# Performance work log

Hardware: AMD Instinct MI355X
Metric: run time of the kernel (lower is better)

## Reference

```python
import jax, jax.numpy as jnp
import numpy as np

B, T, H, D = 1, 2048, 32, 64
SCALE = 0.015625  # 1/64 = 1/head_size
DEG = 2


def setup_inputs() -> dict:
    key = jax.random.key(0)
    k1, k2, k3, k4 = jax.random.split(key, 4)
    q = jax.random.normal(k1, (B, T, H, D), dtype=jnp.float32)
    k = jax.random.normal(k2, (B, T, H, D), dtype=jnp.float32)
    v = jax.random.normal(k3, (B, T, H, D), dtype=jnp.float32)
    # log_G: per-token, per-head log decay (must be <= 0)
    g = -0.1 * jax.random.uniform(k4, (B, T, H), dtype=jnp.float32)
    return {"q": q, "k": k, "v": v, "g": g}


def reference(q, k, v, g):
    # q,k,v: [B,T,H,D]; g: [B,T,H] log-decay (log_G)
    # Power retention, deg=2, attention (quadratic) form for T <= switch_over_seq_len.
    g_cum = jnp.cumsum(g, axis=1)                         # [B,T,H]
    gc = jnp.transpose(g_cum, (0, 2, 1))                  # [B,H,T]
    # decay weight exp(gc[t]-gc[s]) for s<=t, 0 otherwise
    log_decay = gc[:, :, :, None] - gc[:, :, None, :]     # [B,H,T,S]
    causal = jnp.tril(jnp.ones((T, T), dtype=bool))
    decay = jnp.where(causal, jnp.exp(log_decay), 0.0)    # [B,H,T,S]
    qk = jnp.einsum("bthd,bshd->bhts", q, k) * SCALE      # [B,H,T,S]
    w = (qk ** DEG) * decay                               # nonneg scores, deg=2
    num = jnp.einsum("bhts,bshd->bthd", w, v)             # [B,T,H,D]
    denom = jnp.transpose(w.sum(-1), (0, 2, 1))           # [B,T,H]
    out = num / jnp.maximum(denom, 1.0)[..., None]
    return out
```

## Files before the change

kernel.cpp:

```cpp
#include <hip/hip_runtime.h>

#define T_DIM 2048
#define H_DIM 32
#define D_DIM 64
#define SCALE_F 0.015625f
#define TILE_STRIDE 2048

typedef unsigned short ushort;
typedef __attribute__((ext_vector_type(8))) short short8;
typedef __attribute__((ext_vector_type(16))) float f32x16;

__global__ __launch_bounds__(256)
void cumsum_g_kernel(const float* __restrict__ g, float* __restrict__ gc) {
    const int h = blockIdx.x;
    const int tid = threadIdx.x;
    const int PER = T_DIM / 256;

    __shared__ float sums[256];

    float loc[8];
    float run = 0.f;
    const int t0 = tid * PER;
    for (int i = 0; i < PER; ++i) {
        run += g[(size_t)(t0 + i) * H_DIM + h];
        loc[i] = run;
    }
    sums[tid] = run;
    __syncthreads();

    for (int off = 1; off < 256; off <<= 1) {
        float vv = (tid >= off) ? sums[tid - off] : 0.f;
        __syncthreads();
        sums[tid] += vv;
        __syncthreads();
    }
    float excl = (tid == 0) ? 0.f : sums[tid - 1];

    for (int i = 0; i < PER; ++i)
        gc[(size_t)h * T_DIM + t0 + i] = excl + loc[i];
}

__device__ __forceinline__ ushort f2bf(float x) {
    unsigned u = __float_as_uint(x);
    unsigned r = (u + 0x7fffu + ((u >> 16) & 1u)) >> 16;
    return (ushort)r;
}

__global__ __launch_bounds__(256)
void prep_kernel(const float* __restrict__ q, const float* __restrict__ k,
                 const float* __restrict__ v, const float* __restrict__ gc,
                 ushort* __restrict__ qfrag, ushort* __restrict__ kfrag,
                 ushort* __restrict__ vfrag) {
    __shared__ ushort qt_l[64 * 64];
    __shared__ ushort kt_l[64 * 64];

    const int h   = blockIdx.x;
    const int tt  = blockIdx.y;
    const int tid = threadIdx.x;

    {
        const int r    = tid >> 2;
        const int dseg = (tid & 3) * 16;
        const int t    = tt * 64 + r;
        const float gct = gc[(size_t)h * T_DIM + t];
        const float eq = SCALE_F * __expf(0.5f * gct);
        const float ek = __expf(-0.5f * gct);
        const float* qp = q + ((size_t)t * H_DIM + h) * 64 + dseg;
        const float* kp = k + ((size_t)t * H_DIM + h) * 64 + dseg;
        union { ushort u[16]; uint4 uu[2]; } oq, ok;
#pragma unroll
        for (int i = 0; i < 16; ++i) {
            oq.u[i] = f2bf(qp[i] * eq);
            ok.u[i] = f2bf(kp[i] * ek);
        }
        const int c0 = (tid & 3) * 2;
#pragma unroll
        for (int cc = 0; cc < 2; ++cc) {
            const int slot = (c0 + cc) ^ (r & 7);
            *reinterpret_cast<uint4*>(&qt_l[r * 64 + slot * 8]) = oq.uu[cc];
            *reinterpret_cast<uint4*>(&kt_l[r * 64 + slot * 8]) = ok.uu[cc];
        }
    }
    __syncthreads();

#pragma unroll
    for (int n = 0; n < 2; ++n) {
        const int ch   = tid + 256 * n;
        const int l31  = ch & 31;
        const int hi   = (ch >> 5) & 1;
        const int ks   = (ch >> 6) & 3;
        const int t32r = ch >> 8;
        const int row  = t32r * 32 + l31;
        const int slot = (2 * ks + hi) ^ (row & 7);
        uint4 qq = *reinterpret_cast<const uint4*>(&qt_l[row * 64 + slot * 8]);
        uint4 kk = *reinterpret_cast<const uint4*>(&kt_l[row * 64 + slot * 8]);
        const size_t base = ((size_t)h * 64 + tt * 2 + t32r) * TILE_STRIDE
                          + (size_t)(((ks * 2 + hi) * 32) + l31) * 8;
        *reinterpret_cast<uint4*>(qfrag + base) = qq;
        *reinterpret_cast<uint4*>(kfrag + base) = kk;
    }

#pragma unroll
    for (int n = 0; n < 2; ++n) {
        const int c9   = (tid >> 5) + 8 * n;
        const int l31  = tid & 31;
        const int hi   = c9 & 1;
        const int kh2  = (c9 >> 1) & 1;
        const int dblk = (c9 >> 2) & 1;
        const int s32r = c9 >> 3;
        const int tb = tt * 64 + s32r * 32 + kh2 * 16 + hi * 8;
        union { ushort u[8]; uint4 uu; } ov;
#pragma unroll
        for (int j = 0; j < 8; ++j)
            ov.u[j] = f2bf(v[((size_t)(tb + j) * H_DIM + h) * 64 + dblk * 32 + l31]);
        const size_t base = ((size_t)h * 64 + tt * 2 + s32r) * TILE_STRIDE
                          + (size_t)((((dblk * 2 + kh2) * 2 + hi) * 32) + l31) * 8;
        *reinterpret_cast<uint4*>(vfrag + base) = ov.uu;
    }
}

__device__ __forceinline__ short8 ld8(const ushort* p) {
    return *reinterpret_cast<const short8*>(p);
}

__device__ __forceinline__ unsigned cvt_pk_bf16(float lo, float hi) {
    unsigned r;
    asm("v_cvt_pk_bf16_f32 %0, %1, %2" : "=v"(r) : "v"(lo), "v"(hi));
    return r;
}

__device__ __forceinline__ short8 pack_w(const float* w8) {
    unsigned p0 = cvt_pk_bf16(w8[0], w8[1]);
    unsigned p1 = cvt_pk_bf16(w8[2], w8[3]);
    unsigned p2 = cvt_pk_bf16(w8[4], w8[5]);
    unsigned p3 = cvt_pk_bf16(w8[6], w8[7]);
    asm("v_permlane32_swap_b32 %0, %1" : "+v"(p0), "+v"(p2));
    asm("v_permlane32_swap_b32 %0, %1" : "+v"(p1), "+v"(p3));
    union { unsigned u[4]; short8 s; } af;
    af.u[0] = p0; af.u[1] = p1; af.u[2] = p2; af.u[3] = p3;
    return af.s;
}

template<int MODE>
__device__ __forceinline__ void step64(
    const ushort* __restrict__ kb, const ushort* __restrict__ vb,
    int lofs, int hi, int l31,
    const short8 (&qrL)[4], const short8 (&qrH)[4],
    f32x16& o00, f32x16& o01, f32x16& o10, f32x16& o11,
    float& denL, float& denH)
{
    const short8 vf00 = ld8(vb + lofs);
    const short8 vf10 = ld8(vb + 512 + lofs);
    const short8 vf01 = ld8(vb + 1024 + lofs);
    const short8 vf11 = ld8(vb + 1536 + lofs);
    const short8 kf0 = ld8(kb + lofs);
    const short8 kf1 = ld8(kb + 512 + lofs);
    const short8 kf2 = ld8(kb + 1024 + lofs);
    const short8 kf3 = ld8(kb + 1536 + lofs);

    f32x16 cH;
#pragma unroll
    for (int i = 0; i < 16; ++i) cH[i] = 0.f;
    f32x16 cL = cH;

    if (MODE <= 1) {
        cL = __builtin_amdgcn_mfma_f32_32x32x16_bf16(kf0, qrL[0], cL, 0, 0, 0);
        cH = __builtin_amdgcn_mfma_f32_32x32x16_bf16(kf0, qrH[0], cH, 0, 0, 0);
        cL = __builtin_amdgcn_mfma_f32_32x32x16_bf16(kf1, qrL[1], cL, 0, 0, 0);
        cH = __builtin_amdgcn_mfma_f32_32x32x16_bf16(kf1, qrH[1], cH, 0, 0, 0);
        cL = __builtin_amdgcn_mfma_f32_32x32x16_bf16(kf2, qrL[2], cL, 0, 0, 0);
        cH = __builtin_amdgcn_mfma_f32_32x32x16_bf16(kf2, qrH[2], cH, 0, 0, 0);
        cL = __builtin_amdgcn_mfma_f32_32x32x16_bf16(kf3, qrL[3], cL, 0, 0, 0);
        cH = __builtin_amdgcn_mfma_f32_32x32x16_bf16(kf3, qrH[3], cH, 0, 0, 0);
    } else {
        cH = __builtin_amdgcn_mfma_f32_32x32x16_bf16(kf0, qrH[0], cH, 0, 0, 0);
        cH = __builtin_amdgcn_mfma_f32_32x32x16_bf16(kf1, qrH[1], cH, 0, 0, 0);
        cH = __builtin_amdgcn_mfma_f32_32x32x16_bf16(kf2, qrH[2], cH, 0, 0, 0);
        cH = __builtin_amdgcn_mfma_f32_32x32x16_bf16(kf3, qrH[3], cH, 0, 0, 0);
    }

    float wL[16], wH[16];
#pragma unroll
    for (int r = 0; r < 16; ++r) {
        const int s_local = (r & 3) + 8 * (r >> 2) + 4 * hi;
        float xh = cH[r];
        float wwh = xh * xh;
        if (MODE == 2) wwh = (s_local <= l31) ? wwh : 0.f;
        wH[r] = wwh;
        denH += wwh;
        if (MODE <= 1) {
            float xl = cL[r];
            float wwl = xl * xl;
            if (MODE == 1) wwl = (s_local <= l31) ? wwl : 0.f;
            wL[r] = wwl;
            denL += wwl;
        }
    }

    if (MODE <= 1) {
        const short8 a0 = pack_w(&wL[0]);
        o00 = __builtin_amdgcn_mfma_f32_32x32x16_bf16(a0, vf00, o00, 0, 0, 0);
        o01 = __builtin_amdgcn_mfma_f32_32x32x16_bf16(a0, vf01, o01, 0, 0, 0);
        const short8 a1 = pack_w(&wL[8]);
        o00 = __builtin_amdgcn_mfma_f32_32x32x16_bf16(a1, vf10, o00, 0, 0, 0);
        o01 = __builtin_amdgcn_mfma_f32_32x32x16_bf16(a1, vf11, o01, 0, 0, 0);
    }
    {
        const short8 a0 = pack_w(&wH[0]);
        o10 = __builtin_amdgcn_mfma_f32_32x32x16_bf16(a0, vf00, o10, 0, 0, 0);
        o11 = __builtin_amdgcn_mfma_f32_32x32x16_bf16(a0, vf01, o11, 0, 0, 0);
        const short8 a1 = pack_w(&wH[8]);
        o10 = __builtin_amdgcn_mfma_f32_32x32x16_bf16(a1, vf10, o10, 0, 0, 0);
        o11 = __builtin_amdgcn_mfma_f32_32x32x16_bf16(a1, vf11, o11, 0, 0, 0);
    }
}

__device__ __forceinline__ void epi_phase(
    int thalf, const f32x16& od0, const f32x16& od1,
    int t0, int h, int w, int hi, int l31,
    float* __restrict__ out, float* lds_o, const float* lds_den)
{
    __syncthreads();
#pragma unroll
    for (int r = 0; r < 16; ++r) {
        const int row = (r & 3) + 8 * (r >> 2) + 4 * hi;
        lds_o[((w * 2 + 0) * 32 + row) * 32 + l31] = od0[r];
        lds_o[((w * 2 + 1) * 32 + row) * 32 + l31] = od1[r];
    }
    __syncthreads();
#pragma unroll
    for (int rr = 0; rr < 8; ++rr) {
        const int row = 8 * w + rr;
        const float s = lds_o[((0 + hi) * 32 + row) * 32 + l31]
                      + lds_o[((2 + hi) * 32 + row) * 32 + l31]
                      + lds_o[((4 + hi) * 32 + row) * 32 + l31]
                      + lds_o[((6 + hi) * 32 + row) * 32 + l31];
        const float dt = lds_den[(0 + thalf) * 32 + row]
                       + lds_den[(2 + thalf) * 32 + row]
                       + lds_den[(4 + thalf) * 32 + row]
                       + lds_den[(6 + thalf) * 32 + row];
        const float inv = 1.f / fmaxf(dt, 1.f);
        out[((size_t)(t0 + thalf * 32 + row) * H_DIM + h) * 64 + hi * 32 + l31]
            = s * inv;
    }
}

__device__ __forceinline__ void process_tile64(
    int tt, int h, int w, int hi, int l31, int lofs,
    const ushort* __restrict__ qfrag, const ushort* __restrict__ kfrag,
    const ushort* __restrict__ vfrag, float* __restrict__ out,
    float* lds_o, float* lds_den)
{
    short8 qrL[4], qrH[4];
    const ushort* qb = qfrag + ((size_t)h * 64 + 2 * tt) * TILE_STRIDE;
#pragma unroll
    for (int ks = 0; ks < 4; ++ks) {
        qrL[ks] = ld8(qb + ks * 512 + lofs);
        qrH[ks] = ld8(qb + TILE_STRIDE + ks * 512 + lofs);
    }

    f32x16 o00, o01, o10, o11;
#pragma unroll
    for (int i = 0; i < 16; ++i) { o00[i] = 0.f; o01[i] = 0.f; o10[i] = 0.f; o11[i] = 0.f; }
    float denL = 0.f, denH = 0.f;

    const ushort* kh_b = kfrag + (size_t)h * 64 * TILE_STRIDE;
    const ushort* vh_b = vfrag + (size_t)h * 64 * TILE_STRIDE;
    const int dlo = 2 * tt;

    for (int st = w; st < dlo; st += 4)
        step64<0>(kh_b + (size_t)st * TILE_STRIDE, vh_b + (size_t)st * TILE_STRIDE,
                  lofs, hi, l31, qrL, qrH, o00, o01, o10, o11, denL, denH);
    if ((dlo & 3) == w)
        step64<1>(kh_b + (size_t)dlo * TILE_STRIDE, vh_b + (size_t)dlo * TILE_STRIDE,
                  lofs, hi, l31, qrL, qrH, o00, o01, o10, o11, denL, denH);
    if (((dlo + 1) & 3) == w)
        step64<2>(kh_b + (size_t)(dlo + 1) * TILE_STRIDE, vh_b + (size_t)(dlo + 1) * TILE_STRIDE,
                  lofs, hi, l31, qrL, qrH, o00, o01, o10, o11, denL, denH);

    denL += __shfl_xor(denL, 32);
    denH += __shfl_xor(denH, 32);
    if (hi == 0) {
        lds_den[(w * 2 + 0) * 32 + l31] = denL;
        lds_den[(w * 2 + 1) * 32 + l31] = denH;
    }

    const int t0 = tt * 64;
    epi_phase(0, o00, o01, t0, h, w, hi, l31, out, lds_o, lds_den);
    epi_phase(1, o10, o11, t0, h, w, hi, l31, out, lds_o, lds_den);
}

__global__ __launch_bounds__(256, 2)
void retention_mfma_kernel(const ushort* __restrict__ qfrag,
                           const ushort* __restrict__ kfrag,
                           const ushort* __restrict__ vfrag,
                           float* __restrict__ out) {
    __shared__ float lds_o[4 * 2 * 32 * 32];
    __shared__ float lds_den[4 * 2 * 32];

    const int bid = blockIdx.x;
    const int p   = bid >> 5;
    const int h   = bid & 31;
    const int lane = threadIdx.x & 63;
    const int w    = threadIdx.x >> 6;
    const int hi   = lane >> 5;
    const int l31  = lane & 31;
    const int lofs = hi * 256 + l31 * 8;

    process_tile64(31 - p, h, w, hi, l31, lofs, qfrag, kfrag, vfrag, out, lds_o, lds_den);
    process_tile64(p,      h, w, hi, l31, lofs, qfrag, kfrag, vfrag, out, lds_o, lds_den);
}

extern "C" void kernel_launch(void* const* d_in, const int* in_sizes, int n_in,
                              void* d_out, int out_size, void* d_ws, size_t ws_size,
                              hipStream_t stream) {
    const float* q = (const float*)d_in[0];
    const float* k = (const float*)d_in[1];
    const float* v = (const float*)d_in[2];
    const float* g = (const float*)d_in[3];
    float* out = (float*)d_out;

    const size_t GC_BYTES = (size_t)H_DIM * T_DIM * sizeof(float);
    const size_t BF_ELEMS = (size_t)H_DIM * T_DIM * D_DIM;

    float* gc = (float*)d_ws;
    ushort* qfrag = (ushort*)((char*)d_ws + GC_BYTES);
    ushort* kfrag = qfrag + BF_ELEMS;
    ushort* vfrag = kfrag + BF_ELEMS;

    cumsum_g_kernel<<<H_DIM, 256, 0, stream>>>(g, gc);
    prep_kernel<<<dim3(H_DIM, T_DIM / 64), 256, 0, stream>>>(q, k, v, gc,
                                                             qfrag, kfrag, vfrag);
    retention_mfma_kernel<<<16 * H_DIM, 256, 0, stream>>>(qfrag, kfrag, vfrag, out);
}
```

Measured before the change: 45.47 us.

## Double-buffer K/V fragment loads and vectorize squared-weight math with float2

Splits each step into a separate fragment load and compute phase, then software-pipelines the main key loop with two register buffers so the next tile's K/V loads are issued before the current tile's MFMAs run. The squaring and denominator accumulation now use two-wide float vectors, which may let the compiler emit packed FP32 ops. The extra fragment set raises VGPR pressure, which could cause spills or limit occupancy under the 256x2 launch bounds.

```diff
diff --git a/kernel.cpp b/kernel.cpp
--- a/kernel.cpp
+++ b/kernel.cpp
@@ -9,6 +9,7 @@
 typedef unsigned short ushort;
 typedef __attribute__((ext_vector_type(8))) short short8;
 typedef __attribute__((ext_vector_type(16))) float f32x16;
+typedef __attribute__((ext_vector_type(2))) float f32x2;
 
 __global__ __launch_bounds__(256)
 void cumsum_g_kernel(const float* __restrict__ g, float* __restrict__ gc) {
@@ -129,11 +130,11 @@
     return r;
 }
 
-__device__ __forceinline__ short8 pack_w(const float* w8) {
-    unsigned p0 = cvt_pk_bf16(w8[0], w8[1]);
-    unsigned p1 = cvt_pk_bf16(w8[2], w8[3]);
-    unsigned p2 = cvt_pk_bf16(w8[4], w8[5]);
-    unsigned p3 = cvt_pk_bf16(w8[6], w8[7]);
+__device__ __forceinline__ short8 pack_w2(const f32x2* w2) {
+    unsigned p0 = cvt_pk_bf16(w2[0][0], w2[0][1]);
+    unsigned p1 = cvt_pk_bf16(w2[1][0], w2[1][1]);
+    unsigned p2 = cvt_pk_bf16(w2[2][0], w2[2][1]);
+    unsigned p3 = cvt_pk_bf16(w2[3][0], w2[3][1]);
     asm("v_permlane32_swap_b32 %0, %1" : "+v"(p0), "+v"(p2));
     asm("v_permlane32_swap_b32 %0, %1" : "+v"(p1), "+v"(p3));
     union { unsigned u[4]; short8 s; } af;
@@ -141,77 +142,92 @@
     return af.s;
 }
 
+struct Frags {
+    short8 k0, k1, k2, k3;
+    short8 v0, v1, v2, v3;
+};
+
+__device__ __forceinline__ void load_frags(Frags& f, const ushort* kb,
+                                           const ushort* vb, int lofs) {
+    f.v0 = ld8(vb + lofs);
+    f.v1 = ld8(vb + 512 + lofs);
+    f.v2 = ld8(vb + 1024 + lofs);
+    f.v3 = ld8(vb + 1536 + lofs);
+    f.k0 = ld8(kb + lofs);
+    f.k1 = ld8(kb + 512 + lofs);
+    f.k2 = ld8(kb + 1024 + lofs);
+    f.k3 = ld8(kb + 1536 + lofs);
+}
+
 template<int MODE>
-__device__ __forceinline__ void step64(
-    const ushort* __restrict__ kb, const ushort* __restrict__ vb,
-    int lofs, int hi, int l31,
+__device__ __forceinline__ void compute64(
+    const Frags& f, int hi, int l31,
     const short8 (&qrL)[4], const short8 (&qrH)[4],
     f32x16& o00, f32x16& o01, f32x16& o10, f32x16& o11,
-    float& denL, float& denH)
+    f32x2& den2L, f32x2& den2H)
 {
-    const short8 vf00 = ld8(vb + lofs);
-    const short8 vf10 = ld8(vb + 512 + lofs);
-    const short8 vf01 = ld8(vb + 1024 + lofs);
-    const short8 vf11 = ld8(vb + 1536 + lofs);
-    const short8 kf0 = ld8(kb + lofs);
-    const short8 kf1 = ld8(kb + 512 + lofs);
-    const short8 kf2 = ld8(kb + 1024 + lofs);
-    const short8 kf3 = ld8(kb + 1536 + lofs);
-
     f32x16 cH;
 #pragma unroll
     for (int i = 0; i < 16; ++i) cH[i] = 0.f;
     f32x16 cL = cH;
 
     if (MODE <= 1) {
-        cL = __builtin_amdgcn_mfma_f32_32x32x16_bf16(kf0, qrL[0], cL, 0, 0, 0);
-        cH = __builtin_amdgcn_mfma_f32_32x32x16_bf16(kf0, qrH[0], cH, 0, 0, 0);
-        cL = __builtin_amdgcn_mfma_f32_32x32x16_bf16(kf1, qrL[1], cL, 0, 0, 0);
-        cH = __builtin_amdgcn_mfma_f32_32x32x16_bf16(kf1, qrH[1], cH, 0, 0, 0);
-        cL = __builtin_amdgcn_mfma_f32_32x32x16_bf16(kf2, qrL[2], cL, 0, 0, 0);
-        cH = __builtin_amdgcn_mfma_f32_32x32x16_bf16(kf2, qrH[2], cH, 0, 0, 0);
-        cL = __builtin_amdgcn_mfma_f32_32x32x16_bf16(kf3, qrL[3], cL, 0, 0, 0);
-        cH = __builtin_amdgcn_mfma_f32_32x32x16_bf16(kf3, qrH[3], cH, 0, 0, 0);
+        cL = __builtin_amdgcn_mfma_f32_32x32x16_bf16(f.k0, qrL[0], cL, 0, 0, 0);
+        cH = __builtin_amdgcn_mfma_f32_32x32x16_bf16(f.k0, qrH[0], cH, 0, 0, 0);
+        cL = __builtin_amdgcn_mfma_f32_32x32x16_bf16(f.k1, qrL[1], cL, 0, 0, 0);
+        cH = __builtin_amdgcn_mfma_f32_32x32x16_bf16(f.k1, qrH[1], cH, 0, 0, 0);
+        cL = __builtin_amdgcn_mfma_f32_32x32x16_bf16(f.k2, qrL[2], cL, 0, 0, 0);
+        cH = __builtin_amdgcn_mfma_f32_32x32x16_bf16(f.k2, qrH[2], cH, 0, 0, 0);
+        cL = __builtin_amdgcn_mfma_f32_32x32x16_bf16(f.k3, qrL[3], cL, 0, 0, 0);
+        cH = __builtin_amdgcn_mfma_f32_32x32x16_bf16(f.k3, qrH[3], cH, 0, 0, 0);
     } else {
-        cH = __builtin_amdgcn_mfma_f32_32x32x16_bf16(kf0, qrH[0], cH, 0, 0, 0);
-        cH = __builtin_amdgcn_mfma_f32_32x32x16_bf16(kf1, qrH[1], cH, 0, 0, 0);
-        cH = __builtin_amdgcn_mfma_f32_32x32x16_bf16(kf2, qrH[2], cH, 0, 0, 0);
-        cH = __builtin_amdgcn_mfma_f32_32x32x16_bf16(kf3, qrH[3], cH, 0, 0, 0);
-    }
-
-    float wL[16], wH[16];
-#pragma unroll
-    for (int r = 0; r < 16; ++r) {
-        const int s_local = (r & 3) + 8 * (r >> 2) + 4 * hi;
-        float xh = cH[r];
-        float wwh = xh * xh;
-        if (MODE == 2) wwh = (s_local <= l31) ? wwh : 0.f;
-        wH[r] = wwh;
-        denH += wwh;
+        cH = __builtin_amdgcn_mfma_f32_32x32x16_bf16(f.k0, qrH[0], cH, 0, 0, 0);
+        cH = __builtin_amdgcn_mfma_f32_32x32x16_bf16(f.k1, qrH[1], cH, 0, 0, 0);
+        cH = __builtin_amdgcn_mfma_f32_32x32x16_bf16(f.k2, qrH[2], cH, 0, 0, 0);
+        cH = __builtin_amdgcn_mfma_f32_32x32x16_bf16(f.k3, qrH[3], cH, 0, 0, 0);
+    }
+
+    f32x2 wL[8], wH[8];
+#pragma unroll
+    for (int i = 0; i < 8; ++i) {
+        const int r0 = 2 * i, r1 = 2 * i + 1;
+        const int sl0 = (r0 & 3) + 8 * (r0 >> 2) + 4 * hi;
+        const int sl1 = (r1 & 3) + 8 * (r1 >> 2) + 4 * hi;
+        f32x2 x; x[0] = cH[r0]; x[1] = cH[r1];
+        f32x2 ww = x * x;
+        if (MODE == 2) {
+            ww[0] = (sl0 <= l31) ? ww[0] : 0.f;
+            ww[1] = (sl1 <= l31) ? ww[1] : 0.f;
+        }
+        wH[i] = ww;
+        den2H += ww;
         if (MODE <= 1) {
-            float xl = cL[r];
-            float wwl = xl * xl;
-            if (MODE == 1) wwl = (s_local <= l31) ? wwl : 0.f;
-            wL[r] = wwl;
-            denL += wwl;
+            f32x2 y; y[0] = cL[r0]; y[1] = cL[r1];
+            f32x2 wwl = y * y;
+            if (MODE == 1) {
+                wwl[0] = (sl0 <= l31) ? wwl[0] : 0.f;
+                wwl[1] = (sl1 <= l31) ? wwl[1] : 0.f;
+            }
+            wL[i] = wwl;
+            den2L += wwl;
         }
     }
 
     if (MODE <= 1) {
-        const short8 a0 = pack_w(&wL[0]);
-        o00 = __builtin_amdgcn_mfma_f32_32x32x16_bf16(a0, vf00, o00, 0, 0, 0);
-        o01 = __builtin_amdgcn_mfma_f32_32x32x16_bf16(a0, vf01, o01, 0, 0, 0);
-        const short8 a1 = pack_w(&wL[8]);
-        o00 = __builtin_amdgcn_mfma_f32_32x32x16_bf16(a1, vf10, o00, 0, 0, 0);
-        o01 = __builtin_amdgcn_mfma_f32_32x32x16_bf16(a1, vf11, o01, 0, 0, 0);
+        const short8 a0 = pack_w2(&wL[0]);
+        o00 = __builtin_amdgcn_mfma_f32_32x32x16_bf16(a0, f.v0, o00, 0, 0, 0);
+        o01 = __builtin_amdgcn_mfma_f32_32x32x16_bf16(a0, f.v2, o01, 0, 0, 0);
+        const short8 a1 = pack_w2(&wL[4]);
+        o00 = __builtin_amdgcn_mfma_f32_32x32x16_bf16(a1, f.v1, o00, 0, 0, 0);
+        o01 = __builtin_amdgcn_mfma_f32_32x32x16_bf16(a1, f.v3, o01, 0, 0, 0);
     }
     {
-        const short8 a0 = pack_w(&wH[0]);
-        o10 = __builtin_amdgcn_mfma_f32_32x32x16_bf16(a0, vf00, o10, 0, 0, 0);
-        o11 = __builtin_amdgcn_mfma_f32_32x32x16_bf16(a0, vf01, o11, 0, 0, 0);
-        const short8 a1 = pack_w(&wH[8]);
-        o10 = __builtin_amdgcn_mfma_f32_32x32x16_bf16(a1, vf10, o10, 0, 0, 0);
-        o11 = __builtin_amdgcn_mfma_f32_32x32x16_bf16(a1, vf11, o11, 0, 0, 0);
+        const short8 b0 = pack_w2(&wH[0]);
+        o10 = __builtin_amdgcn_mfma_f32_32x32x16_bf16(b0, f.v0, o10, 0, 0, 0);
+        o11 = __builtin_amdgcn_mfma_f32_32x32x16_bf16(b0, f.v2, o11, 0, 0, 0);
+        const short8 b1 = pack_w2(&wH[4]);
+        o10 = __builtin_amdgcn_mfma_f32_32x32x16_bf16(b1, f.v1, o10, 0, 0, 0);
+        o11 = __builtin_amdgcn_mfma_f32_32x32x16_bf16(b1, f.v3, o11, 0, 0, 0);
     }
 }
 
@@ -262,22 +278,41 @@
     f32x16 o00, o01, o10, o11;
 #pragma unroll
     for (int i = 0; i < 16; ++i) { o00[i] = 0.f; o01[i] = 0.f; o10[i] = 0.f; o11[i] = 0.f; }
-    float denL = 0.f, denH = 0.f;
+    f32x2 den2L, den2H;
+    den2L[0] = 0.f; den2L[1] = 0.f; den2H[0] = 0.f; den2H[1] = 0.f;
 
     const ushort* kh_b = kfrag + (size_t)h * 64 * TILE_STRIDE;
     const ushort* vh_b = vfrag + (size_t)h * 64 * TILE_STRIDE;
     const int dlo = 2 * tt;
 
-    for (int st = w; st < dlo; st += 4)
-        step64<0>(kh_b + (size_t)st * TILE_STRIDE, vh_b + (size_t)st * TILE_STRIDE,
-                  lofs, hi, l31, qrL, qrH, o00, o01, o10, o11, denL, denH);
-    if ((dlo & 3) == w)
-        step64<1>(kh_b + (size_t)dlo * TILE_STRIDE, vh_b + (size_t)dlo * TILE_STRIDE,
-                  lofs, hi, l31, qrL, qrH, o00, o01, o10, o11, denL, denH);
-    if (((dlo + 1) & 3) == w)
-        step64<2>(kh_b + (size_t)(dlo + 1) * TILE_STRIDE, vh_b + (size_t)(dlo + 1) * TILE_STRIDE,
-                  lofs, hi, l31, qrL, qrH, o00, o01, o10, o11, denL, denH);
-
+    Frags fA, fB;
+    int st = w;
+    if (st < dlo)
+        load_frags(fA, kh_b + (size_t)st * TILE_STRIDE, vh_b + (size_t)st * TILE_STRIDE, lofs);
+    for (; st + 4 < dlo; st += 8) {
+        load_frags(fB, kh_b + (size_t)(st + 4) * TILE_STRIDE,
+                   vh_b + (size_t)(st + 4) * TILE_STRIDE, lofs);
+        compute64<0>(fA, hi, l31, qrL, qrH, o00, o01, o10, o11, den2L, den2H);
+        if (st + 8 < dlo)
+            load_frags(fA, kh_b + (size_t)(st + 8) * TILE_STRIDE,
+                       vh_b + (size_t)(st + 8) * TILE_STRIDE, lofs);
+        compute64<0>(fB, hi, l31, qrL, qrH, o00, o01, o10, o11, den2L, den2H);
+    }
+    if (st < dlo)
+        compute64<0>(fA, hi, l31, qrL, qrH, o00, o01, o10, o11, den2L, den2H);
+
+    if ((dlo & 3) == w) {
+        load_frags(fA, kh_b + (size_t)dlo * TILE_STRIDE, vh_b + (size_t)dlo * TILE_STRIDE, lofs);
+        compute64<1>(fA, hi, l31, qrL, qrH, o00, o01, o10, o11, den2L, den2H);
+    }
+    if (((dlo + 1) & 3) == w) {
+        load_frags(fA, kh_b + (size_t)(dlo + 1) * TILE_STRIDE,
+                   vh_b + (size_t)(dlo + 1) * TILE_STRIDE, lofs);
+        compute64<2>(fA, hi, l31, qrL, qrH, o00, o01, o10, o11, den2L, den2H);
+    }
+
+    float denL = den2L[0] + den2L[1];
+    float denH = den2H[0] + den2H[1];
     denL += __shfl_xor(denL, 32);
     denH += __shfl_xor(denH, 32);
     if (hi == 0) {
```

New measurement: 46.61 us. 1.03x slower.
